# Performance work log

Measured on AMD Instinct MI355X. Metric: run time of the kernel, lower is better.

The kernel has to match this reference:

```python
import jax, jax.numpy as jnp
import numpy as np


def fps(p, m):
    """Furthest point sampling. p: (B,N,3) -> idx (B,m) int32. Starts at index 0 like pointops."""
    p = jax.lax.stop_gradient(p)
    B, N, _ = p.shape
    d2 = jnp.full((B, N), jnp.inf, dtype=p.dtype)  # min sq-dist to selected set
    first = jnp.zeros((B,), dtype=jnp.int32)

    def step(carry, _):
        d2, last = carry
        lastp = jnp.take_along_axis(p, last[:, None, None].astype(jnp.int32), axis=1)  # (B,1,3)
        dist = jnp.sum((p - lastp) ** 2, axis=-1)  # (B,N)
        d2 = jnp.minimum(d2, dist)
        nxt = jnp.argmax(d2, axis=-1).astype(jnp.int32)
        return (d2, nxt), last

    _, idx = jax.lax.scan(step, (d2, first), None, length=m)
    return jnp.transpose(idx)  # (B,m)


def knn_indices(p1, p2, k):
    """k nearest neighbors of p2 (B,M,3) among p1 (B,N,3) -> (B,M,k) int32."""
    p1 = jax.lax.stop_gradient(p1)
    p2 = jax.lax.stop_gradient(p2)
    # squared distances (B,M,N)
    d2 = (jnp.sum(p2 ** 2, -1)[:, :, None]
          + jnp.sum(p1 ** 2, -1)[:, None, :]
          - 2.0 * jnp.einsum('bmd,bnd->bmn', p2, p1))
    _, idx = jax.lax.top_k(-d2, k)
    return idx.astype(jnp.int32)


def setup_inputs() -> dict:
    key = jax.random.key(0)
    k1, k2 = jax.random.split(key)
    B, N, C = 8, 8192, 64
    p1 = jax.random.normal(k1, (B, N, 3), dtype=jnp.float32)
    x = jax.random.normal(k2, (B, N, C), dtype=jnp.float32)
    return {"p1": p1, "x": x, "stride": 4, "num_neighbors": 16}


def reference(p1, x, stride, num_neighbors):
    B, N, C = x.shape
    M = N // stride
    idx = fps(p1, M)                                   # (B,M) int32
    p2 = jnp.take_along_axis(p1, idx[:, :, None], 1)   # (B,M,3) sampled coords
    nn = knn_indices(p1, p2, num_neighbors)            # (B,M,k)
    # gather features: (B,M,k,C)
    grouped = jax.vmap(lambda xb, ib: xb[ib])(x, nn)
    y = jnp.mean(grouped, axis=2)                      # (B,M,C)
    return (y, p2, idx)
```

## Files before the change

kernel.cpp:

```cpp
#include <hip/hip_runtime.h>

#define Bn 8
#define Nn 8192
#define Cn 64
#define Mn 2048
#define Kn 16
#define FPS_T 512
#define PPT (Nn / FPS_T)
#define NPAIR (PPT / 2)

typedef float f32x2 __attribute__((ext_vector_type(2)));
typedef unsigned long long u64;

template <int CTRL, int RMASK>
__device__ __forceinline__ float dpp_max_step(float v) {
    int mv = __builtin_amdgcn_update_dpp(__float_as_int(v), __float_as_int(v),
                                         CTRL, RMASK, 0xF, false);
    return fmaxf(v, __int_as_float(mv));
}
template <int CTRL, int RMASK>
__device__ __forceinline__ unsigned dpp_min_step(unsigned v) {
    unsigned mv = (unsigned)__builtin_amdgcn_update_dpp((int)v, (int)v,
                                                        CTRL, RMASK, 0xF, false);
    return (mv < v) ? mv : v;
}
__device__ __forceinline__ float wave_max_f32(float v) {
    v = dpp_max_step<0x111, 0xF>(v);
    v = dpp_max_step<0x112, 0xF>(v);
    v = dpp_max_step<0x114, 0xF>(v);
    v = dpp_max_step<0x118, 0xF>(v);
    v = dpp_max_step<0x142, 0xA>(v);
    v = dpp_max_step<0x143, 0xC>(v);
    return v;
}
__device__ __forceinline__ unsigned wave_min_u32(unsigned v) {
    v = dpp_min_step<0x111, 0xF>(v);
    v = dpp_min_step<0x112, 0xF>(v);
    v = dpp_min_step<0x114, 0xF>(v);
    v = dpp_min_step<0x118, 0xF>(v);
    v = dpp_min_step<0x142, 0xA>(v);
    v = dpp_min_step<0x143, 0xC>(v);
    return v;
}
__device__ __forceinline__ u64 u64max(u64 a, u64 b) { return a > b ? a : b; }

__global__ __launch_bounds__(FPS_T) void fps_kernel(
    const float* __restrict__ p1,
    float* __restrict__ out_p2,
    float* __restrict__ out_idxf)
{
#pragma clang fp contract(off)
    __shared__ float s_Px[Nn], s_Py[Nn], s_Pz[Nn];
    __shared__ u64 s_wkey[2][8];
    __shared__ int s_oidx[Mn];

    const int b = blockIdx.x;
    const int t = threadIdx.x;
    const int w = t >> 6;
    const float* __restrict__ P = p1 + (size_t)b * (Nn * 3);

    f32x2 px2[NPAIR], py2[NPAIR], pz2[NPAIR], d2v[NPAIR];
#pragma unroll
    for (int j = 0; j < PPT; ++j) {
        const int g = t + j * FPS_T;
        const float x = P[g * 3 + 0];
        const float y = P[g * 3 + 1];
        const float z = P[g * 3 + 2];
        const int k = j >> 1;
        if ((j & 1) == 0) { px2[k].x = x; py2[k].x = y; pz2[k].x = z; d2v[k].x = __int_as_float(0x7f800000); }
        else              { px2[k].y = x; py2[k].y = y; pz2[k].y = z; d2v[k].y = __int_as_float(0x7f800000); }
        s_Px[g] = x; s_Py[g] = y; s_Pz[g] = z;
    }
    if (t == 0) s_oidx[0] = 0;
    __syncthreads();

    float qx = s_Px[0], qy = s_Py[0], qz = s_Pz[0];

    for (int m = 1; m < Mn; ++m) {
#pragma clang fp contract(off)
        const f32x2 nqx = { -qx, -qx };
        const f32x2 nqy = { -qy, -qy };
        const f32x2 nqz = { -qz, -qz };
        float lm = -1.0f;
#pragma unroll
        for (int k = 0; k < NPAIR; ++k) {
            const f32x2 dx = px2[k] + nqx;
            const f32x2 dy = py2[k] + nqy;
            const f32x2 dz = pz2[k] + nqz;
            const f32x2 mx = dx * dx;
            const f32x2 my = dy * dy;
            const f32x2 mz = dz * dz;
            const f32x2 s  = (mx + my) + mz;
            const float nlo = fminf(d2v[k].x, s.x);
            const float nhi = fminf(d2v[k].y, s.y);
            d2v[k].x = nlo;
            d2v[k].y = nhi;
            lm = fmaxf(lm, nlo);
            lm = fmaxf(lm, nhi);
        }
        lm = wave_max_f32(lm);
        const float V = __int_as_float(
            __builtin_amdgcn_readlane(__float_as_int(lm), 63));
        unsigned cand = 0xFFFFFFFFu;
#pragma unroll
        for (int k = NPAIR - 1; k >= 0; --k) {
            const unsigned ghi = (unsigned)(t + (2 * k + 1) * FPS_T);
            const unsigned glo = (unsigned)(t + (2 * k) * FPS_T);
            cand = (d2v[k].y == V) ? ghi : cand;
            cand = (d2v[k].x == V) ? glo : cand;
        }
        cand = wave_min_u32(cand);
        if ((t & 63) == 63) {
            const u64 key = ((u64)(unsigned)__float_as_int(V) << 32) |
                            (u64)(~cand);
            s_wkey[m & 1][w] = key;
        }
        __syncthreads();
        const u64* __restrict__ K = s_wkey[m & 1];
        const u64 a0 = u64max(K[0], K[1]);
        const u64 a1 = u64max(K[2], K[3]);
        const u64 a2 = u64max(K[4], K[5]);
        const u64 a3 = u64max(K[6], K[7]);
        const u64 kk = u64max(u64max(a0, a1), u64max(a2, a3));
        const int bi = (int)(~(unsigned)kk);
        if (t == 0) s_oidx[m] = bi;
        qx = s_Px[bi]; qy = s_Py[bi]; qz = s_Pz[bi];
    }
    __syncthreads();

    float* __restrict__ o2 = out_p2 + (size_t)b * Mn * 3;
    float* __restrict__ oi = out_idxf + (size_t)b * Mn;
    for (int i = t; i < Mn; i += FPS_T) {
        const int bi = s_oidx[i];
        oi[i] = (float)bi;
        o2[i * 3 + 0] = s_Px[bi];
        o2[i * 3 + 1] = s_Py[bi];
        o2[i * 3 + 2] = s_Pz[bi];
    }
}

#define KNN_WPB 4
__global__ __launch_bounds__(64 * KNN_WPB) void knn_mean_kernel(
    const float* __restrict__ p1,
    const float* __restrict__ x,
    const float* __restrict__ p2,
    float* __restrict__ y)
{
    const int lane = threadIdx.x & 63;
    const int wid  = threadIdx.x >> 6;
    const int q    = blockIdx.x * KNN_WPB + wid;
    const int b    = q >> 11;
    const float* __restrict__ P = p1 + (size_t)b * (Nn * 3);

    const float qx = p2[(size_t)q * 3 + 0];
    const float qy = p2[(size_t)q * 3 + 1];
    const float qz = p2[(size_t)q * 3 + 2];
    const float qq = __fadd_rn(
        __fadd_rn(__fmul_rn(qx, qx), __fmul_rn(qy, qy)), __fmul_rn(qz, qz));

    float slotv = __int_as_float(0x7f800000);
    int   sloti = 0x7fffffff;
    float thr   = __int_as_float(0x7f800000);
    int   thri  = 0x7fffffff;

    for (int c = 0; c < Nn / 64; ++c) {
        const int g = c * 64 + lane;
        const float ax = P[g * 3 + 0];
        const float ay = P[g * 3 + 1];
        const float az = P[g * 3 + 2];
        const float pp = __fadd_rn(
            __fadd_rn(__fmul_rn(ax, ax), __fmul_rn(ay, ay)), __fmul_rn(az, az));
        const float dot = __fmaf_rn(az, qz, __fmaf_rn(ay, qy, __fmul_rn(ax, qx)));
        const float d = __fsub_rn(__fadd_rn(qq, pp), __fmul_rn(2.0f, dot));
        const bool pass = (d < thr) || (d == thr && g < thri);
        unsigned long long ball = __ballot(pass);
        while (ball) {
            const int src = __builtin_ctzll(ball);
            ball &= ball - 1ull;
            const float v  = __shfl(d, src);
            const int   vi = __shfl(g, src);
            const float upv = __shfl_up(slotv, 1);
            const int   upi = __shfl_up(sloti, 1);
            const bool beforeme = (v < slotv) || (v == slotv && vi < sloti);
            bool beforeup = (v < upv) || (v == upv && vi < upi);
            if (lane == 0) beforeup = false;
            if (beforeme) {
                slotv = beforeup ? upv : v;
                sloti = beforeup ? upi : vi;
            }
            thr  = __shfl(slotv, 15);
            thri = __shfl(sloti, 15);
        }
    }

    float acc = 0.0f;
    const float* __restrict__ xb = x + (size_t)b * Nn * Cn;
#pragma unroll
    for (int s = 0; s < Kn; ++s) {
        const int ni = __shfl(sloti, s);
        acc = __fadd_rn(acc, xb[(size_t)ni * Cn + lane]);
    }
    y[(size_t)q * Cn + lane] = __fmul_rn(acc, 0.0625f);
}

extern "C" void kernel_launch(void* const* d_in, const int* in_sizes, int n_in,
                              void* d_out, int out_size, void* d_ws, size_t ws_size,
                              hipStream_t stream) {
    const float* p1 = (const float*)d_in[0];
    const float* x  = (const float*)d_in[1];

    float* y    = (float*)d_out;
    float* p2   = y    + (size_t)Bn * Mn * Cn;
    float* idxf = p2   + (size_t)Bn * Mn * 3;

    fps_kernel<<<Bn, FPS_T, 0, stream>>>(p1, p2, idxf);
    knn_mean_kernel<<<(Bn * Mn) / KNN_WPB, 64 * KNN_WPB, 0, stream>>>(p1, x, p2, y);
}
```

Before: 2.117 ms.

## Halve FPS block size, inline packed-math asm, skip candidate scan for non-max lanes

New measurement: 2.663 ms. 25.8% more time.

```diff
diff --git a/kernel.cpp b/kernel.cpp
--- a/kernel.cpp
+++ b/kernel.cpp
@@ -5,9 +5,10 @@
 #define Cn 64
 #define Mn 2048
 #define Kn 16
-#define FPS_T 512
+#define FPS_T 256
 #define PPT (Nn / FPS_T)
 #define NPAIR (PPT / 2)
+#define NWAVE (FPS_T / 64)
 
 typedef float f32x2 __attribute__((ext_vector_type(2)));
 typedef unsigned long long u64;
@@ -44,14 +45,13 @@
 }
 __device__ __forceinline__ u64 u64max(u64 a, u64 b) { return a > b ? a : b; }
 
-__global__ __launch_bounds__(FPS_T) void fps_kernel(
+__global__ __launch_bounds__(FPS_T, 1) void fps_kernel(
     const float* __restrict__ p1,
     float* __restrict__ out_p2,
     float* __restrict__ out_idxf)
 {
-#pragma clang fp contract(off)
     __shared__ float s_Px[Nn], s_Py[Nn], s_Pz[Nn];
-    __shared__ u64 s_wkey[2][8];
+    __shared__ u64 s_wkey[2][NWAVE];
     __shared__ int s_oidx[Mn];
 
     const int b = blockIdx.x;
@@ -59,7 +59,8 @@
     const int w = t >> 6;
     const float* __restrict__ P = p1 + (size_t)b * (Nn * 3);
 
-    f32x2 px2[NPAIR], py2[NPAIR], pz2[NPAIR], d2v[NPAIR];
+    f32x2 px2[NPAIR], py2[NPAIR], pz2[NPAIR];
+    float d2lo[NPAIR], d2hi[NPAIR];
 #pragma unroll
     for (int j = 0; j < PPT; ++j) {
         const int g = t + j * FPS_T;
@@ -67,9 +68,14 @@
         const float y = P[g * 3 + 1];
         const float z = P[g * 3 + 2];
         const int k = j >> 1;
-        if ((j & 1) == 0) { px2[k].x = x; py2[k].x = y; pz2[k].x = z; d2v[k].x = __int_as_float(0x7f800000); }
-        else              { px2[k].y = x; py2[k].y = y; pz2[k].y = z; d2v[k].y = __int_as_float(0x7f800000); }
+        if ((j & 1) == 0) { px2[k].x = x; py2[k].x = y; pz2[k].x = z; }
+        else              { px2[k].y = x; py2[k].y = y; pz2[k].y = z; }
         s_Px[g] = x; s_Py[g] = y; s_Pz[g] = z;
+    }
+#pragma unroll
+    for (int k = 0; k < NPAIR; ++k) {
+        d2lo[k] = __int_as_float(0x7f800000);
+        d2hi[k] = __int_as_float(0x7f800000);
     }
     if (t == 0) s_oidx[0] = 0;
     __syncthreads();
@@ -77,37 +83,42 @@
     float qx = s_Px[0], qy = s_Py[0], qz = s_Pz[0];
 
     for (int m = 1; m < Mn; ++m) {
-#pragma clang fp contract(off)
         const f32x2 nqx = { -qx, -qx };
         const f32x2 nqy = { -qy, -qy };
         const f32x2 nqz = { -qz, -qz };
         float lm = -1.0f;
 #pragma unroll
         for (int k = 0; k < NPAIR; ++k) {
-            const f32x2 dx = px2[k] + nqx;
-            const f32x2 dy = py2[k] + nqy;
-            const f32x2 dz = pz2[k] + nqz;
-            const f32x2 mx = dx * dx;
-            const f32x2 my = dy * dy;
-            const f32x2 mz = dz * dz;
-            const f32x2 s  = (mx + my) + mz;
-            const float nlo = fminf(d2v[k].x, s.x);
-            const float nhi = fminf(d2v[k].y, s.y);
-            d2v[k].x = nlo;
-            d2v[k].y = nhi;
-            lm = fmaxf(lm, nlo);
-            lm = fmaxf(lm, nhi);
-        }
-        lm = wave_max_f32(lm);
+            f32x2 s, t1, t2;
+            asm("v_pk_add_f32 %0, %3, %6\n\t"
+                "v_pk_add_f32 %1, %4, %7\n\t"
+                "v_pk_add_f32 %2, %5, %8\n\t"
+                "v_pk_mul_f32 %0, %0, %0\n\t"
+                "v_pk_mul_f32 %1, %1, %1\n\t"
+                "v_pk_mul_f32 %2, %2, %2\n\t"
+                "v_pk_add_f32 %0, %0, %1\n\t"
+                "v_pk_add_f32 %0, %0, %2"
+                : "=&v"(s), "=&v"(t1), "=&v"(t2)
+                : "v"(px2[k]), "v"(py2[k]), "v"(pz2[k]),
+                  "v"(nqx), "v"(nqy), "v"(nqz));
+            const float nlo = fminf(d2lo[k], s.x);
+            const float nhi = fminf(d2hi[k], s.y);
+            d2lo[k] = nlo;
+            d2hi[k] = nhi;
+            lm = fmaxf(lm, fmaxf(nlo, nhi));
+        }
+        const float wv = wave_max_f32(lm);
         const float V = __int_as_float(
-            __builtin_amdgcn_readlane(__float_as_int(lm), 63));
+            __builtin_amdgcn_readlane(__float_as_int(wv), 63));
         unsigned cand = 0xFFFFFFFFu;
-#pragma unroll
-        for (int k = NPAIR - 1; k >= 0; --k) {
-            const unsigned ghi = (unsigned)(t + (2 * k + 1) * FPS_T);
-            const unsigned glo = (unsigned)(t + (2 * k) * FPS_T);
-            cand = (d2v[k].y == V) ? ghi : cand;
-            cand = (d2v[k].x == V) ? glo : cand;
+        if (lm == V) {
+#pragma unroll
+            for (int k = NPAIR - 1; k >= 0; --k) {
+                const unsigned ghi = (unsigned)(t + (2 * k + 1) * FPS_T);
+                const unsigned glo = (unsigned)(t + (2 * k) * FPS_T);
+                cand = (d2hi[k] == V) ? ghi : cand;
+                cand = (d2lo[k] == V) ? glo : cand;
+            }
         }
         cand = wave_min_u32(cand);
         if ((t & 63) == 63) {
@@ -117,11 +128,7 @@
         }
         __syncthreads();
         const u64* __restrict__ K = s_wkey[m & 1];
-        const u64 a0 = u64max(K[0], K[1]);
-        const u64 a1 = u64max(K[2], K[3]);
-        const u64 a2 = u64max(K[4], K[5]);
-        const u64 a3 = u64max(K[6], K[7]);
-        const u64 kk = u64max(u64max(a0, a1), u64max(a2, a3));
+        const u64 kk = u64max(u64max(K[0], K[1]), u64max(K[2], K[3]));
         const int bi = (int)(~(unsigned)kk);
         if (t == 0) s_oidx[m] = bi;
         qx = s_Px[bi]; qy = s_Py[bi]; qz = s_Pz[bi];
```

## Speculate per-lane argmax and broadcast winning coords via wave DPP reduction

Applied to the files above, without the earlier changes.

Result: slower. 2.229 ms (+5.3%).

```diff
diff --git a/kernel.cpp b/kernel.cpp
--- a/kernel.cpp
+++ b/kernel.cpp
@@ -8,9 +8,11 @@
 #define FPS_T 512
 #define PPT (Nn / FPS_T)
 #define NPAIR (PPT / 2)
+#define NWAVE 8
 
 typedef float f32x2 __attribute__((ext_vector_type(2)));
 typedef unsigned long long u64;
+typedef unsigned u32;
 
 template <int CTRL, int RMASK>
 __device__ __forceinline__ float dpp_max_step(float v) {
@@ -42,7 +44,19 @@
     v = dpp_min_step<0x143, 0xC>(v);
     return v;
 }
-__device__ __forceinline__ u64 u64max(u64 a, u64 b) { return a > b ? a : b; }
+template <int CTRL, int RMASK>
+__device__ __forceinline__ void dpp_kmax_step(u32& hi, u32& lo) {
+    const u32 h2 = (u32)__builtin_amdgcn_update_dpp((int)hi, (int)hi, CTRL, RMASK, 0xF, false);
+    const u32 l2 = (u32)__builtin_amdgcn_update_dpp((int)lo, (int)lo, CTRL, RMASK, 0xF, false);
+    const u64 a  = ((u64)hi << 32) | lo;
+    const u64 b2 = ((u64)h2 << 32) | l2;
+    if (b2 > a) { hi = h2; lo = l2; }
+}
+__device__ __forceinline__ void kmax8(u32& hi, u32& lo) {
+    dpp_kmax_step<0x111, 0xF>(hi, lo);
+    dpp_kmax_step<0x112, 0xF>(hi, lo);
+    dpp_kmax_step<0x114, 0xF>(hi, lo);
+}
 
 __global__ __launch_bounds__(FPS_T) void fps_kernel(
     const float* __restrict__ p1,
@@ -51,12 +65,13 @@
 {
 #pragma clang fp contract(off)
     __shared__ float s_Px[Nn], s_Py[Nn], s_Pz[Nn];
-    __shared__ u64 s_wkey[2][8];
+    __shared__ u32 s_slot[2][NWAVE][8];
     __shared__ int s_oidx[Mn];
 
     const int b = blockIdx.x;
     const int t = threadIdx.x;
     const int w = t >> 6;
+    const int lane = t & 63;
     const float* __restrict__ P = p1 + (size_t)b * (Nn * 3);
 
     f32x2 px2[NPAIR], py2[NPAIR], pz2[NPAIR], d2v[NPAIR];
@@ -95,36 +110,47 @@
             const float nhi = fminf(d2v[k].y, s.y);
             d2v[k].x = nlo;
             d2v[k].y = nhi;
-            lm = fmaxf(lm, nlo);
-            lm = fmaxf(lm, nhi);
-        }
-        lm = wave_max_f32(lm);
+            lm = fmaxf(lm, fmaxf(nlo, nhi));
+        }
+        u32 spec = 0xFFFFFFFFu;
+#pragma unroll
+        for (int k = NPAIR - 1; k >= 0; --k) {
+            const u32 ghi = (u32)(t + (2 * k + 1) * FPS_T);
+            const u32 glo = (u32)(t + (2 * k) * FPS_T);
+            spec = (d2v[k].y == lm) ? ghi : spec;
+            spec = (d2v[k].x == lm) ? glo : spec;
+        }
+        const float wv = wave_max_f32(lm);
         const float V = __int_as_float(
-            __builtin_amdgcn_readlane(__float_as_int(lm), 63));
-        unsigned cand = 0xFFFFFFFFu;
-#pragma unroll
-        for (int k = NPAIR - 1; k >= 0; --k) {
-            const unsigned ghi = (unsigned)(t + (2 * k + 1) * FPS_T);
-            const unsigned glo = (unsigned)(t + (2 * k) * FPS_T);
-            cand = (d2v[k].y == V) ? ghi : cand;
-            cand = (d2v[k].x == V) ? glo : cand;
-        }
+            __builtin_amdgcn_readlane(__float_as_int(wv), 63));
+        u32 cand = (lm == V) ? spec : 0xFFFFFFFFu;
         cand = wave_min_u32(cand);
-        if ((t & 63) == 63) {
-            const u64 key = ((u64)(unsigned)__float_as_int(V) << 32) |
-                            (u64)(~cand);
-            s_wkey[m & 1][w] = key;
+        if (lane == 63) {
+            const u32 g = cand;
+            u32* sl = (u32*)&s_slot[m & 1][w][0];
+            sl[0] = __float_as_uint(V);
+            sl[1] = (~g) & 0x1FFFu;
+            sl[2] = __float_as_uint(s_Px[g]);
+            sl[3] = __float_as_uint(s_Py[g]);
+            sl[4] = __float_as_uint(s_Pz[g]);
         }
         __syncthreads();
-        const u64* __restrict__ K = s_wkey[m & 1];
-        const u64 a0 = u64max(K[0], K[1]);
-        const u64 a1 = u64max(K[2], K[3]);
-        const u64 a2 = u64max(K[4], K[5]);
-        const u64 a3 = u64max(K[6], K[7]);
-        const u64 kk = u64max(u64max(a0, a1), u64max(a2, a3));
-        const int bi = (int)(~(unsigned)kk);
-        if (t == 0) s_oidx[m] = bi;
-        qx = s_Px[bi]; qy = s_Py[bi]; qz = s_Pz[bi];
+        const u32* base = (const u32*)&s_slot[m & 1][lane & 7][0];
+        const u32 k0 = base[0];
+        const u32 k1 = base[1];
+        const u32 cx = base[2];
+        const u32 cy = base[3];
+        const u32 cz = base[4];
+        u32 hi = k0, lo = k1;
+        kmax8(hi, lo);
+        const u32 sV  = (u32)__builtin_amdgcn_readlane((int)hi, 7);
+        const u32 sNG = (u32)__builtin_amdgcn_readlane((int)lo, 7);
+        const bool win = (k0 == sV) && (k1 == sNG);
+        const int ls = (int)__builtin_ctzll(__ballot(win));
+        qx = __uint_as_float((u32)__builtin_amdgcn_readlane((int)cx, ls));
+        qy = __uint_as_float((u32)__builtin_amdgcn_readlane((int)cy, ls));
+        qz = __uint_as_float((u32)__builtin_amdgcn_readlane((int)cz, ls));
+        if (t == 0) s_oidx[m] = (int)((~sNG) & 0x1FFFu);
     }
     __syncthreads();
 
```
